# Performance work log

Hardware: AMD Instinct MI355X
Metric: run time of the kernel (lower is better)

## Reference

```python
import jax, jax.numpy as jnp
import numpy as np

NEG_SLOPE = 0.2  # PyG GATConv default


def leaky_relu(v):
    return jnp.where(v >= 0, v, NEG_SLOPE * v)


def gat_conv(x, W, a_src, a_dst, b, src, dst, n_nodes):
    # x: [N, Fin], W: [Fin, Fout], a_src/a_dst/b: [Fout]
    h = x @ W                               # [N, Fout]
    alpha_src = h @ a_src                   # [N]
    alpha_dst = h @ a_dst                   # [N]
    e = leaky_relu(alpha_src[src] + alpha_dst[dst])          # [E]
    m = jax.ops.segment_max(e, dst, num_segments=n_nodes)    # [N] (self-loops => every node has >=1 edge)
    p = jnp.exp(e - m[dst])                                   # [E]
    s = jax.ops.segment_sum(p, dst, num_segments=n_nodes)     # [N]
    coef = p / s[dst]                                          # [E]
    out = jax.ops.segment_sum(coef[:, None] * h[src], dst, num_segments=n_nodes)
    return out + b


def setup_inputs() -> dict:
    key = jax.random.key(0)
    ks = jax.random.split(key, 20)
    N, E, DIN, DH, DOUT, G = 50000, 800000, 128, 256, 2, 512
    x = jax.random.normal(ks[0], (N, DIN), dtype=jnp.float32)
    edge_index = jax.random.randint(ks[1], (2, E), 0, N, dtype=jnp.int64)
    batch = jnp.sort(jax.random.randint(ks[2], (N,), 0, G, dtype=jnp.int64))

    def lin(k, fin, fout):
        return jax.random.normal(k, (fin, fout), dtype=jnp.float32) * (1.0 / np.sqrt(fin))

    def att(k, f):
        return jax.random.normal(k, (f,), dtype=jnp.float32) * (1.0 / np.sqrt(f))

    return {
        "x": x, "edge_index": edge_index, "batch": batch,
        "W1": lin(ks[3], DIN, DH), "as1": att(ks[4], DH), "ad1": att(ks[5], DH), "b1": jnp.zeros((DH,), jnp.float32),
        "W2": lin(ks[6], DH, DH),  "as2": att(ks[7], DH), "ad2": att(ks[8], DH), "b2": jnp.zeros((DH,), jnp.float32),
        "W3": lin(ks[9], DH, DH),  "as3": att(ks[10], DH), "ad3": att(ks[11], DH), "b3": jnp.zeros((DH,), jnp.float32),
        "Wfc": lin(ks[12], DH, DOUT), "bfc": jnp.zeros((DOUT,), jnp.float32),
    }


def reference(x, edge_index, batch, W1, as1, ad1, b1, W2, as2, ad2, b2, W3, as3, ad3, b3, Wfc, bfc):
    N = x.shape[0]
    G = 512  # number of graphs (static)
    # add self-loops (PyG GATConv default add_self_loops=True)
    loops = jnp.arange(N, dtype=edge_index.dtype)
    src = jnp.concatenate([edge_index[0], loops])
    dst = jnp.concatenate([edge_index[1], loops])

    h = jax.nn.relu(gat_conv(x, W1, as1, ad1, b1, src, dst, N))
    h = jax.nn.relu(gat_conv(h, W2, as2, ad2, b2, src, dst, N))
    h = jax.nn.relu(gat_conv(h, W3, as3, ad3, b3, src, dst, N))

    # global mean pool over graphs
    sums = jax.ops.segment_sum(h, batch, num_segments=G)                 # [G, DH]
    counts = jax.ops.segment_sum(jnp.ones((N,), h.dtype), batch, num_segments=G)
    pooled = sums / jnp.maximum(counts, 1.0)[:, None]

    logits = pooled @ Wfc + bfc                                           # [G, DOUT]
    return jax.nn.softmax(logits, axis=1)
```

## Files before the change

### kernel.cpp

```cpp
#include <hip/hip_runtime.h>
#include <hip/hip_bf16.h>

typedef short short8 __attribute__((ext_vector_type(8)));
typedef float floatx4 __attribute__((ext_vector_type(4)));
typedef float float2v __attribute__((ext_vector_type(2)));
typedef unsigned short ushort_t;
typedef unsigned short ushort4v __attribute__((ext_vector_type(4)));

__device__ __forceinline__ ushort_t f2bf(float v) {
    __hip_bfloat16 h = __float2bfloat16(v);
    return *(ushort_t*)&h;
}
__device__ __forceinline__ float bf2f(ushort_t u) {
    return __uint_as_float(((unsigned)u) << 16);
}

#if defined(__has_builtin)
#if __has_builtin(__builtin_amdgcn_cvt_pk_f32_fp8) && __has_builtin(__builtin_amdgcn_cvt_pk_fp8_f32)
#define HAVE_FP8_CVT 1
#endif
#endif

__device__ __forceinline__ unsigned enc_fp8(float f) {
    unsigned t = __float_as_uint(f);
    unsigned s = (t >> 24) & 0x80u;
    unsigned mag = t & 0x7fffffffu;
    if (mag > 0x43E00000u) mag = 0x43E00000u;
    mag += 0x7FFFFu + ((mag >> 20) & 1u);
    int e = (int)(mag >> 20) - 960;
    unsigned r = (e < 1) ? 0u : (unsigned)e;
    return s | r;
}
__device__ __forceinline__ float dec_fp8(unsigned b) {
    unsigned bits = ((b & 0x80u) << 24) | ((b & 0x7fu) << 20);
    return __uint_as_float(bits) * 0x1p120f;
}

__device__ __forceinline__ unsigned pack4_fp8(float a, float b, float c, float d) {
#if HAVE_FP8_CVT
    unsigned v = 0;
    v = __builtin_amdgcn_cvt_pk_fp8_f32(a, b, v, false);
    v = __builtin_amdgcn_cvt_pk_fp8_f32(c, d, v, true);
    return v;
#else
    return enc_fp8(a) | (enc_fp8(b) << 8) | (enc_fp8(c) << 16) | (enc_fp8(d) << 24);
#endif
}
__device__ __forceinline__ float4 unpack4_fp8(unsigned v) {
#if HAVE_FP8_CVT
    float2v lo = __builtin_amdgcn_cvt_pk_f32_fp8(v, false);
    float2v hi = __builtin_amdgcn_cvt_pk_f32_fp8(v, true);
    return make_float4(lo.x, lo.y, hi.x, hi.y);
#else
    return make_float4(dec_fp8(v & 0xFFu), dec_fp8((v >> 8) & 0xFFu),
                       dec_fp8((v >> 16) & 0xFFu), dec_fp8(v >> 24));
#endif
}


template <int NCSHIFT>
__device__ __forceinline__ void wsplit_coal(const float* __restrict__ W,
                                            ushort_t* __restrict__ Bh,
                                            ushort_t* __restrict__ Bl,
                                            int o, bool permK) {
    int j = o & 7;
    int l = (o >> 3) & 63;
    int rest = o >> 9;
    int nt = rest >> NCSHIFT;
    int c  = rest & ((1 << NCSHIFT) - 1);
    int n  = nt * 16 + (l & 15);
    int ks = c * 32 + (l >> 4) * 8 + j;
    int i = ks & 63;
    int ko = permK ? ((ks & ~63) | ((i & 3) << 4) | (i >> 2)) : ks;
    float v = W[(size_t)ko * 256 + n];
    ushort_t h = f2bf(v);
    Bh[o] = h;
    Bl[o] = f2bf(v - bf2f(h));
}

__global__ __launch_bounds__(256) void prep_kernel(const float* __restrict__ X,
                                                   ushort_t* __restrict__ Xhi,
                                                   ushort_t* __restrict__ Xlo,
                                                   int* __restrict__ deg,
                                                   float* __restrict__ asrcA,
                                                   float* __restrict__ adstA,
                                                   const float* __restrict__ W1,
                                                   const float* __restrict__ W2,
                                                   const float* __restrict__ W3,
                                                   ushort_t* __restrict__ B1h, ushort_t* __restrict__ B1l,
                                                   ushort_t* __restrict__ B2h, ushort_t* __restrict__ B2l,
                                                   ushort_t* __restrict__ B3h, ushort_t* __restrict__ B3l,
                                                   int total, int N) {
    int idx = blockIdx.x * 256 + threadIdx.x;
    if (idx < N) {
        deg[idx] = 0;
        asrcA[idx] = 0.f;
        adstA[idx] = 0.f;
    }
    const int S1 = 128 * 256, S2 = 256 * 256;
    if (idx < S1) {
        wsplit_coal<2>(W1, B1h, B1l, idx, false);
    } else if (idx < S1 + S2) {
        wsplit_coal<3>(W2, B2h, B2l, idx - S1, true);
    } else if (idx < S1 + 2 * S2) {
        wsplit_coal<3>(W3, B3h, B3l, idx - S1 - S2, true);
    }
    if (idx < total) {
        float v = X[idx];
        ushort_t h = f2bf(v);
        Xhi[idx] = h;
        Xlo[idx] = f2bf(v - bf2f(h));
    }
}

template <int NCHUNK, bool HASLO>
__global__ __launch_bounds__(256) void gemm_mfma(const ushort_t* __restrict__ Ahi_g,
                                                 const ushort_t* __restrict__ Alo_g,
                                                 const ushort_t* __restrict__ Bthi,
                                                 const ushort_t* __restrict__ Btlo,
                                                 unsigned char* __restrict__ Hb,
                                                 const float* __restrict__ a_src,
                                                 const float* __restrict__ a_dst,
                                                 float* __restrict__ asrc_out,
                                                 float* __restrict__ adst_out,
                                                 int N) {
    constexpr int K = NCHUNK * 32;
    const int tid = threadIdx.x;
    const int wave = tid >> 6, lane = tid & 63;
    const int wr = wave & 1, wc = wave >> 1;
    const int q = lane >> 4, l15 = lane & 15;
    const int rowBase = blockIdx.x * 128;
    const int colBase = blockIdx.y * 128;

    floatx4 acc[4][4];
#pragma unroll
    for (int i = 0; i < 4; ++i)
#pragma unroll
        for (int j = 0; j < 4; ++j) acc[i][j] = (floatx4)0.f;

    size_t aoff[4];
#pragma unroll
    for (int mt = 0; mt < 4; ++mt) {
        int r = rowBase + wr * 64 + mt * 16 + l15;
        if (r > N - 1) r = N - 1;
        aoff[mt] = (size_t)r * K + q * 8;
    }

    const int ntg = blockIdx.y * 8 + wc * 4;
    const size_t ntstride = (size_t)NCHUNK * 512;
    const ushort_t* bhp = Bthi + (size_t)ntg * ntstride + (size_t)lane * 8;
    const ushort_t* blp = Btlo + (size_t)ntg * ntstride + (size_t)lane * 8;

#pragma unroll
    for (int c = 0; c < NCHUNK; ++c) {
        const int co = c * 32;
        const size_t cb = (size_t)c * 512;
        short8 ah[4], al[4], bh[4], bl[4];
#pragma unroll
        for (int mt = 0; mt < 4; ++mt)
            ah[mt] = *(const short8*)(Ahi_g + aoff[mt] + co);
        if (HASLO) {
#pragma unroll
            for (int mt = 0; mt < 4; ++mt)
                al[mt] = *(const short8*)(Alo_g + aoff[mt] + co);
        }
#pragma unroll
        for (int nt = 0; nt < 4; ++nt) {
            bh[nt] = *(const short8*)(bhp + (size_t)nt * ntstride + cb);
            bl[nt] = *(const short8*)(blp + (size_t)nt * ntstride + cb);
        }
#pragma unroll
        for (int mt = 0; mt < 4; ++mt)
#pragma unroll
            for (int nt = 0; nt < 4; ++nt) {
                acc[mt][nt] = __builtin_amdgcn_mfma_f32_16x16x32_bf16(ah[mt], bh[nt], acc[mt][nt], 0, 0, 0);
                acc[mt][nt] = __builtin_amdgcn_mfma_f32_16x16x32_bf16(ah[mt], bl[nt], acc[mt][nt], 0, 0, 0);
            }
        if (HASLO) {
#pragma unroll
            for (int mt = 0; mt < 4; ++mt)
#pragma unroll
                for (int nt = 0; nt < 4; ++nt)
                    acc[mt][nt] = __builtin_amdgcn_mfma_f32_16x16x32_bf16(al[mt], bh[nt], acc[mt][nt], 0, 0, 0);
        }
    }

    float asv[4], adv[4];
#pragma unroll
    for (int nt = 0; nt < 4; ++nt) {
        int n = colBase + wc * 64 + nt * 16 + l15;
        asv[nt] = a_src[n];
        adv[nt] = a_dst[n];
    }
#pragma unroll
    for (int mt = 0; mt < 4; ++mt) {
#pragma unroll
        for (int reg = 0; reg < 4; ++reg) {
            int grow = rowBase + wr * 64 + mt * 16 + q * 4 + reg;
            float p1 = acc[mt][0][reg] * asv[0] + acc[mt][1][reg] * asv[1] +
                       acc[mt][2][reg] * asv[2] + acc[mt][3][reg] * asv[3];
            float p2 = acc[mt][0][reg] * adv[0] + acc[mt][1][reg] * adv[1] +
                       acc[mt][2][reg] * adv[2] + acc[mt][3][reg] * adv[3];
            if (grow < N) {
                unsigned pk = pack4_fp8(acc[mt][0][reg], acc[mt][1][reg],
                                        acc[mt][2][reg], acc[mt][3][reg]);
                *(unsigned*)(Hb + (size_t)grow * 256 + colBase + wc * 64 + l15 * 4) = pk;
            }
#pragma unroll
            for (int off = 1; off < 16; off <<= 1) {
                p1 += __shfl_xor(p1, off, 64);
                p2 += __shfl_xor(p2, off, 64);
            }
            if (l15 == 0 && grow < N) {
                atomicAdd(&asrc_out[grow], p1);
                atomicAdd(&adst_out[grow], p2);
            }
        }
    }
}

__global__ __launch_bounds__(256) void count_kernel(const int* __restrict__ edst,
                                                    int* __restrict__ deg, int E) {
    int i = blockIdx.x * 256 + threadIdx.x;
    if (i < E) atomicAdd(&deg[edst[i]], 1);
}

__global__ __launch_bounds__(256) void scan1_kernel(const int* __restrict__ deg,
                                                    int* __restrict__ excl,
                                                    int* __restrict__ bsum, int N) {
    __shared__ int tmp[256];
    int tid = threadIdx.x;
    int i = blockIdx.x * 256 + tid;
    int v = (i < N) ? deg[i] : 0;
    tmp[tid] = v;
    __syncthreads();
    for (int off = 1; off < 256; off <<= 1) {
        int t = (tid >= off) ? tmp[tid - off] : 0;
        __syncthreads();
        tmp[tid] += t;
        __syncthreads();
    }
    if (i < N) excl[i] = tmp[tid] - v;
    if (tid == 255) bsum[blockIdx.x] = tmp[255];
}

__global__ __launch_bounds__(256) void scan2_kernel(int* __restrict__ bsum, int nb) {
    __shared__ int tmp[256];
    int tid = threadIdx.x;
    int v = (tid < nb) ? bsum[tid] : 0;
    tmp[tid] = v;
    __syncthreads();
    for (int off = 1; off < 256; off <<= 1) {
        int t = (tid >= off) ? tmp[tid - off] : 0;
        __syncthreads();
        tmp[tid] += t;
        __syncthreads();
    }
    if (tid < nb) bsum[tid] = tmp[tid] - v;
}

__global__ __launch_bounds__(256) void scan3_kernel(const int* __restrict__ excl,
                                                    const int* __restrict__ bsum,
                                                    int* __restrict__ rowptr,
                                                    int* __restrict__ cursor,
                                                    int N, int E) {
    int i = blockIdx.x * 256 + threadIdx.x;
    if (i < N) {
        int v = excl[i] + bsum[blockIdx.x];
        rowptr[i] = v;
        cursor[i] = v;
    }
    if (i == 0) rowptr[N] = E;
}

__global__ __launch_bounds__(256) void scatter_kernel(const int* __restrict__ esrc,
                                                      const int* __restrict__ edst,
                                                      int* __restrict__ cursor,
                                                      int* __restrict__ csr_src, int E) {
    int i = blockIdx.x * 256 + threadIdx.x;
    if (i < E) {
        int d = edst[i];
        int pos = atomicAdd(&cursor[d], 1);
        csr_src[pos] = esrc[i];
    }
}

__global__ __launch_bounds__(256) void gat_fused_kernel(const unsigned char* __restrict__ hb,
                                                        const float* __restrict__ asrc,
                                                        const float* __restrict__ adst,
                                                        const int* __restrict__ rowptr,
                                                        const int* __restrict__ csr_src,
                                                        const float* __restrict__ bias,
                                                        ushort_t* __restrict__ ohi,
                                                        float* __restrict__ asrc_next,
                                                        float* __restrict__ adst_next,
                                                        int N) {
    int wave = threadIdx.x >> 6;
    int lane = threadIdx.x & 63;
    int d = blockIdx.x * 4 + wave;
    if (d >= N) return;

    if (lane == 0) {
        asrc_next[d] = 0.f;
        adst_next[d] = 0.f;
    }

    const float* bb = bias + (lane >> 4) * 64 + (lane & 15);
    float b0 = bb[0], b1 = bb[16], b2 = bb[32], b3 = bb[48];

    float ad = adst[d];
    float es = asrc[d] + ad;
    es = es >= 0.f ? es : 0.2f * es;
    float m = es;
    float s = 1.0f;
    float4 acc = unpack4_fp8(*(const unsigned*)(hb + (size_t)d * 256 + lane * 4));

    int beg = rowptr[d], end = rowptr[d + 1];
    for (int base = beg; base < end; base += 64) {
        int cnt = min(64, end - base);
        int srci = 0;
        float e = -1e30f;
        if (lane < cnt) {
            srci = csr_src[base + lane];
            float v = asrc[srci] + ad;
            e = v >= 0.f ? v : 0.2f * v;
        }
        float cm = e;
#pragma unroll
        for (int off = 32; off > 0; off >>= 1) cm = fmaxf(cm, __shfl_xor(cm, off, 64));
        float mnew = fmaxf(m, cm);
        float scale = __expf(m - mnew);
        m = mnew;

        float p = __expf(e - m);
        float ps = p;
#pragma unroll
        for (int off = 32; off > 0; off >>= 1) ps += __shfl_xor(ps, off, 64);
        s = s * scale + ps;
        acc.x *= scale; acc.y *= scale; acc.z *= scale; acc.w *= scale;

        int j = 0;
        for (; j + 4 <= cnt; j += 4) {
            float p0 = __shfl(p, j, 64),     p1 = __shfl(p, j + 1, 64);
            float p2 = __shfl(p, j + 2, 64), p3 = __shfl(p, j + 3, 64);
            int s0 = __shfl(srci, j, 64),     s1i = __shfl(srci, j + 1, 64);
            int s2i = __shfl(srci, j + 2, 64), s3i = __shfl(srci, j + 3, 64);
            unsigned v0 = *(const unsigned*)(hb + (size_t)s0 * 256 + lane * 4);
            unsigned v1 = *(const unsigned*)(hb + (size_t)s1i * 256 + lane * 4);
            unsigned v2 = *(const unsigned*)(hb + (size_t)s2i * 256 + lane * 4);
            unsigned v3 = *(const unsigned*)(hb + (size_t)s3i * 256 + lane * 4);
            float4 hv0 = unpack4_fp8(v0);
            float4 hv1 = unpack4_fp8(v1);
            float4 hv2 = unpack4_fp8(v2);
            float4 hv3 = unpack4_fp8(v3);
            acc.x += p0 * hv0.x + p1 * hv1.x + p2 * hv2.x + p3 * hv3.x;
            acc.y += p0 * hv0.y + p1 * hv1.y + p2 * hv2.y + p3 * hv3.y;
            acc.z += p0 * hv0.z + p1 * hv1.z + p2 * hv2.z + p3 * hv3.z;
            acc.w += p0 * hv0.w + p1 * hv1.w + p2 * hv2.w + p3 * hv3.w;
        }
        for (; j < cnt; ++j) {
            float pj = __shfl(p, j, 64);
            int sj = __shfl(srci, j, 64);
            float4 hv = unpack4_fp8(*(const unsigned*)(hb + (size_t)sj * 256 + lane * 4));
            acc.x += pj * hv.x; acc.y += pj * hv.y; acc.z += pj * hv.z; acc.w += pj * hv.w;
        }
    }
    float inv = 1.0f / s;
    float ox = fmaxf(acc.x * inv + b0, 0.f);
    float oy = fmaxf(acc.y * inv + b1, 0.f);
    float oz = fmaxf(acc.z * inv + b2, 0.f);
    float ow = fmaxf(acc.w * inv + b3, 0.f);
    ushort4v hv;
    hv.x = f2bf(ox); hv.y = f2bf(oy); hv.z = f2bf(oz); hv.w = f2bf(ow);
    *(ushort4v*)(ohi + (size_t)d * 256 + lane * 4) = hv;
}

__device__ __forceinline__ int lower_bound_i(const int* __restrict__ a, int n, int v) {
    int lo = 0, hi = n;
    while (lo < hi) {
        int mid = (lo + hi) >> 1;
        if (a[mid] < v) lo = mid + 1; else hi = mid;
    }
    return lo;
}

__global__ __launch_bounds__(256) void pool_fc_kernel(const ushort_t* __restrict__ hhi,
                                                      const int* __restrict__ batch,
                                                      int N,
                                                      const float* __restrict__ Wfc,
                                                      const float* __restrict__ bfc,
                                                      float* __restrict__ out) {
    __shared__ float red0[256];
    __shared__ float red1[256];
    int g = blockIdx.x;
    int c = threadIdx.x;
    int i = c & 63;
    int o = (c & ~63) | ((i & 3) << 4) | (i >> 2);
    int beg = lower_bound_i(batch, N, g);
    int end = lower_bound_i(batch, N, g + 1);
    float sum = 0.f;
    for (int n = beg; n < end; ++n)
        sum += bf2f(hhi[(size_t)n * 256 + c]);
    float cnt = (float)(end - beg);
    float v = sum / fmaxf(cnt, 1.0f);
    red0[c] = v * Wfc[o * 2 + 0];
    red1[c] = v * Wfc[o * 2 + 1];
    __syncthreads();
    for (int off = 128; off > 0; off >>= 1) {
        if (c < off) {
            red0[c] += red0[c + off];
            red1[c] += red1[c + off];
        }
        __syncthreads();
    }
    if (c == 0) {
        float l0 = red0[0] + bfc[0];
        float l1 = red1[0] + bfc[1];
        float mx = fmaxf(l0, l1);
        float e0 = expf(l0 - mx), e1 = expf(l1 - mx);
        float s = e0 + e1;
        out[g * 2 + 0] = e0 / s;
        out[g * 2 + 1] = e1 / s;
    }
}

extern "C" void kernel_launch(void* const* d_in, const int* in_sizes, int n_in,
                              void* d_out, int out_size, void* d_ws, size_t ws_size,
                              hipStream_t stream) {
    const float* x    = (const float*)d_in[0];
    const int*   eidx = (const int*)d_in[1];
    const int*   batch= (const int*)d_in[2];
    const float* Wl[3]  = {(const float*)d_in[3], (const float*)d_in[7],  (const float*)d_in[11]};
    const float* asl[3] = {(const float*)d_in[4], (const float*)d_in[8],  (const float*)d_in[12]};
    const float* adl[3] = {(const float*)d_in[5], (const float*)d_in[9],  (const float*)d_in[13]};
    const float* bl[3]  = {(const float*)d_in[6], (const float*)d_in[10], (const float*)d_in[14]};
    const float* Wfc = (const float*)d_in[15];
    const float* bfc = (const float*)d_in[16];
    float* out = (float*)d_out;

    const int N   = in_sizes[2];
    const int E   = in_sizes[1] / 2;
    const int DIN = in_sizes[0] / N;
    const int DH  = 256;
    const int G   = 512;
    const int* esrc = eidx;
    const int* edst = eidx + E;

    char* ws = (char*)d_ws;
    size_t off = 0;
    const size_t featHalf = (size_t)N * DH * sizeof(ushort_t);
    unsigned char* hb = (unsigned char*)(ws + off); off += (size_t)N * DH;
    ushort_t* ghi    = (ushort_t*)(ws + off); off += featHalf;
    ushort_t* xhi    = (ushort_t*)(ws + off); off += (size_t)N * DIN * sizeof(ushort_t);
    ushort_t* xlo    = (ushort_t*)(ws + off); off += (size_t)N * DIN * sizeof(ushort_t);
    float*    asA    = (float*)(ws + off); off += (size_t)N * sizeof(float);
    float*    adA    = (float*)(ws + off); off += (size_t)N * sizeof(float);
    float*    asB    = (float*)(ws + off); off += (size_t)N * sizeof(float);
    float*    adB    = (float*)(ws + off); off += (size_t)N * sizeof(float);
    int*      deg    = (int*)(ws + off);   off += (size_t)N * sizeof(int);
    int*      excl   = (int*)(ws + off);   off += (size_t)N * sizeof(int);
    int*      rowptr = (int*)(ws + off);   off += (size_t)(N + 1) * sizeof(int);
    int*      cursor = (int*)(ws + off);   off += (size_t)N * sizeof(int);
    int*      bsum   = (int*)(ws + off);   off += 1024;
    int*      csrsrc = (int*)(ws + off);   off += (size_t)E * sizeof(int);
    ushort_t* B1h    = (ushort_t*)(ws + off); off += (size_t)128 * 256 * sizeof(ushort_t);
    ushort_t* B1l    = (ushort_t*)(ws + off); off += (size_t)128 * 256 * sizeof(ushort_t);
    ushort_t* B2h    = (ushort_t*)(ws + off); off += (size_t)256 * 256 * sizeof(ushort_t);
    ushort_t* B2l    = (ushort_t*)(ws + off); off += (size_t)256 * 256 * sizeof(ushort_t);
    ushort_t* B3h    = (ushort_t*)(ws + off); off += (size_t)256 * 256 * sizeof(ushort_t);
    ushort_t* B3l    = (ushort_t*)(ws + off); off += (size_t)256 * 256 * sizeof(ushort_t);

    const int nbN = (N + 255) / 256;

    prep_kernel<<<((size_t)N * DIN + 255) / 256, 256, 0, stream>>>(
        x, xhi, xlo, deg, asA, adA, Wl[0], Wl[1], Wl[2],
        B1h, B1l, B2h, B2l, B3h, B3l, N * DIN, N);

    count_kernel<<<(E + 255) / 256, 256, 0, stream>>>(edst, deg, E);
    scan1_kernel<<<nbN, 256, 0, stream>>>(deg, excl, bsum, N);
    scan2_kernel<<<1, 256, 0, stream>>>(bsum, nbN);
    scan3_kernel<<<nbN, 256, 0, stream>>>(excl, bsum, rowptr, cursor, N, E);
    scatter_kernel<<<(E + 255) / 256, 256, 0, stream>>>(esrc, edst, cursor, csrsrc, E);

    const ushort_t* Bh[3]  = {B1h, B2h, B3h};
    const ushort_t* Blp[3] = {B1l, B2l, B3l};
    float* asCur[3] = {asA, asB, asA};
    float* adCur[3] = {adA, adB, adA};
    float* asNext[3] = {asB, asA, asB};
    float* adNext[3] = {adB, adA, adB};

    dim3 ggrid((N + 127) / 128, 2);
    for (int layer = 0; layer < 3; ++layer) {
        if (layer == 0) {
            gemm_mfma<4, true><<<ggrid, 256, 0, stream>>>(xhi, xlo, Bh[0], Blp[0], hb,
                                                          asl[0], adl[0], asCur[0], adCur[0], N);
        } else {
            gemm_mfma<8, false><<<ggrid, 256, 0, stream>>>(ghi, nullptr, Bh[layer], Blp[layer], hb,
                                                           asl[layer], adl[layer],
                                                           asCur[layer], adCur[layer], N);
        }

        gat_fused_kernel<<<(N + 3) / 4, 256, 0, stream>>>(hb, asCur[layer], adCur[layer],
                                                          rowptr, csrsrc, bl[layer], ghi,
                                                          asNext[layer], adNext[layer], N);
    }

    pool_fc_kernel<<<G, 256, 0, stream>>>(ghi, batch, N, Wfc, bfc, out);
}
```

Baseline: 448.8 us.

## Bucket edges before CSR scatter, fold degree count into prep, drop B-lo MFMAs

```diff
diff --git a/kernel.cpp b/kernel.cpp
--- a/kernel.cpp
+++ b/kernel.cpp
@@ -82,6 +82,9 @@
                                                    ushort_t* __restrict__ Xhi,
                                                    ushort_t* __restrict__ Xlo,
                                                    int* __restrict__ deg,
+                                                   int* __restrict__ bcnt,
+                                                   const int* __restrict__ edst,
+                                                   int E,
                                                    float* __restrict__ asrcA,
                                                    float* __restrict__ adstA,
                                                    const float* __restrict__ W1,
@@ -93,9 +96,13 @@
                                                    int total, int N) {
     int idx = blockIdx.x * 256 + threadIdx.x;
     if (idx < N) {
-        deg[idx] = 0;
         asrcA[idx] = 0.f;
         adstA[idx] = 0.f;
+    }
+    if (idx < E) {
+        int d = edst[idx];
+        atomicAdd(&deg[d], 1);
+        atomicAdd(&bcnt[d >> 7], 1);
     }
     const int S1 = 128 * 256, S2 = 256 * 256;
     if (idx < S1) {
@@ -113,7 +120,7 @@
     }
 }
 
-template <int NCHUNK, bool HASLO>
+template <int NCHUNK, bool ALO, bool BLO>
 __global__ __launch_bounds__(256) void gemm_mfma(const ushort_t* __restrict__ Ahi_g,
                                                  const ushort_t* __restrict__ Alo_g,
                                                  const ushort_t* __restrict__ Bthi,
@@ -159,7 +166,7 @@
 #pragma unroll
         for (int mt = 0; mt < 4; ++mt)
             ah[mt] = *(const short8*)(Ahi_g + aoff[mt] + co);
-        if (HASLO) {
+        if (ALO) {
 #pragma unroll
             for (int mt = 0; mt < 4; ++mt)
                 al[mt] = *(const short8*)(Alo_g + aoff[mt] + co);
@@ -167,22 +174,18 @@
 #pragma unroll
         for (int nt = 0; nt < 4; ++nt) {
             bh[nt] = *(const short8*)(bhp + (size_t)nt * ntstride + cb);
-            bl[nt] = *(const short8*)(blp + (size_t)nt * ntstride + cb);
+            if (BLO) bl[nt] = *(const short8*)(blp + (size_t)nt * ntstride + cb);
         }
 #pragma unroll
         for (int mt = 0; mt < 4; ++mt)
 #pragma unroll
             for (int nt = 0; nt < 4; ++nt) {
                 acc[mt][nt] = __builtin_amdgcn_mfma_f32_16x16x32_bf16(ah[mt], bh[nt], acc[mt][nt], 0, 0, 0);
-                acc[mt][nt] = __builtin_amdgcn_mfma_f32_16x16x32_bf16(ah[mt], bl[nt], acc[mt][nt], 0, 0, 0);
+                if (BLO)
+                    acc[mt][nt] = __builtin_amdgcn_mfma_f32_16x16x32_bf16(ah[mt], bl[nt], acc[mt][nt], 0, 0, 0);
+                if (ALO)
+                    acc[mt][nt] = __builtin_amdgcn_mfma_f32_16x16x32_bf16(al[mt], bh[nt], acc[mt][nt], 0, 0, 0);
             }
-        if (HASLO) {
-#pragma unroll
-            for (int mt = 0; mt < 4; ++mt)
-#pragma unroll
-                for (int nt = 0; nt < 4; ++nt)
-                    acc[mt][nt] = __builtin_amdgcn_mfma_f32_16x16x32_bf16(al[mt], bh[nt], acc[mt][nt], 0, 0, 0);
-        }
     }
 
     float asv[4], adv[4];
@@ -219,12 +222,6 @@
     }
 }
 
-__global__ __launch_bounds__(256) void count_kernel(const int* __restrict__ edst,
-                                                    int* __restrict__ deg, int E) {
-    int i = blockIdx.x * 256 + threadIdx.x;
-    if (i < E) atomicAdd(&deg[edst[i]], 1);
-}
-
 __global__ __launch_bounds__(256) void scan1_kernel(const int* __restrict__ deg,
                                                     int* __restrict__ excl,
                                                     int* __restrict__ bsum, int N) {
@@ -273,15 +270,42 @@
     if (i == 0) rowptr[N] = E;
 }
 
-__global__ __launch_bounds__(256) void scatter_kernel(const int* __restrict__ esrc,
-                                                      const int* __restrict__ edst,
-                                                      int* __restrict__ cursor,
-                                                      int* __restrict__ csr_src, int E) {
+__global__ __launch_bounds__(512) void bscan_kernel(int* __restrict__ bcnt,
+                                                    int* __restrict__ bcur, int nb) {
+    __shared__ int tmp[512];
+    int tid = threadIdx.x;
+    int v = (tid < nb) ? bcnt[tid] : 0;
+    tmp[tid] = v;
+    __syncthreads();
+    for (int off = 1; off < 512; off <<= 1) {
+        int t = (tid >= off) ? tmp[tid - off] : 0;
+        __syncthreads();
+        tmp[tid] += t;
+        __syncthreads();
+    }
+    if (tid < nb) bcur[tid] = tmp[tid] - v;
+}
+
+__global__ __launch_bounds__(256) void bucket_scatter_kernel(const int* __restrict__ esrc,
+                                                             const int* __restrict__ edst,
+                                                             int* __restrict__ bcur,
+                                                             uint2* __restrict__ ebuf, int E) {
     int i = blockIdx.x * 256 + threadIdx.x;
     if (i < E) {
-        int d = edst[i];
-        int pos = atomicAdd(&cursor[d], 1);
-        csr_src[pos] = esrc[i];
+        int s = esrc[i], d = edst[i];
+        int pos = atomicAdd(&bcur[d >> 7], 1);
+        ebuf[pos] = make_uint2((unsigned)s, (unsigned)d);
+    }
+}
+
+__global__ __launch_bounds__(256) void final_scatter_kernel(const uint2* __restrict__ ebuf,
+                                                            int* __restrict__ cursor,
+                                                            int* __restrict__ csr_src, int E) {
+    int i = blockIdx.x * 256 + threadIdx.x;
+    if (i < E) {
+        uint2 e = ebuf[i];
+        int pos = atomicAdd(&cursor[e.y], 1);
+        csr_src[pos] = (int)e.x;
     }
 }
 
@@ -443,6 +467,7 @@
     const int DIN = in_sizes[0] / N;
     const int DH  = 256;
     const int G   = 512;
+    const int NB  = (N + 127) >> 7;
     const int* esrc = eidx;
     const int* edst = eidx + E;
 
@@ -462,7 +487,10 @@
     int*      rowptr = (int*)(ws + off);   off += (size_t)(N + 1) * sizeof(int);
     int*      cursor = (int*)(ws + off);   off += (size_t)N * sizeof(int);
     int*      bsum   = (int*)(ws + off);   off += 1024;
+    int*      bcnt   = (int*)(ws + off);   off += 2048;
+    int*      bcur   = (int*)(ws + off);   off += 2048;
     int*      csrsrc = (int*)(ws + off);   off += (size_t)E * sizeof(int);
+    uint2*    ebuf   = (uint2*)(ws + off); off += (size_t)E * sizeof(uint2);
     ushort_t* B1h    = (ushort_t*)(ws + off); off += (size_t)128 * 256 * sizeof(ushort_t);
     ushort_t* B1l    = (ushort_t*)(ws + off); off += (size_t)128 * 256 * sizeof(ushort_t);
     ushort_t* B2h    = (ushort_t*)(ws + off); off += (size_t)256 * 256 * sizeof(ushort_t);
@@ -472,15 +500,18 @@
 
     const int nbN = (N + 255) / 256;
 
+    hipMemsetAsync(deg, 0, (size_t)N * sizeof(int), stream);
+    hipMemsetAsync(bcnt, 0, (size_t)NB * sizeof(int), stream);
     prep_kernel<<<((size_t)N * DIN + 255) / 256, 256, 0, stream>>>(
-        x, xhi, xlo, deg, asA, adA, Wl[0], Wl[1], Wl[2],
+        x, xhi, xlo, deg, bcnt, edst, E, asA, adA, Wl[0], Wl[1], Wl[2],
         B1h, B1l, B2h, B2l, B3h, B3l, N * DIN, N);
 
-    count_kernel<<<(E + 255) / 256, 256, 0, stream>>>(edst, deg, E);
     scan1_kernel<<<nbN, 256, 0, stream>>>(deg, excl, bsum, N);
     scan2_kernel<<<1, 256, 0, stream>>>(bsum, nbN);
     scan3_kernel<<<nbN, 256, 0, stream>>>(excl, bsum, rowptr, cursor, N, E);
-    scatter_kernel<<<(E + 255) / 256, 256, 0, stream>>>(esrc, edst, cursor, csrsrc, E);
+    bscan_kernel<<<1, 512, 0, stream>>>(bcnt, bcur, NB);
+    bucket_scatter_kernel<<<(E + 255) / 256, 256, 0, stream>>>(esrc, edst, bcur, ebuf, E);
+    final_scatter_kernel<<<(E + 255) / 256, 256, 0, stream>>>(ebuf, cursor, csrsrc, E);
 
     const ushort_t* Bh[3]  = {B1h, B2h, B3h};
     const ushort_t* Blp[3] = {B1l, B2l, B3l};
@@ -492,12 +523,12 @@
     dim3 ggrid((N + 127) / 128, 2);
     for (int layer = 0; layer < 3; ++layer) {
         if (layer == 0) {
-            gemm_mfma<4, true><<<ggrid, 256, 0, stream>>>(xhi, xlo, Bh[0], Blp[0], hb,
-                                                          asl[0], adl[0], asCur[0], adCur[0], N);
+            gemm_mfma<4, true, true><<<ggrid, 256, 0, stream>>>(xhi, xlo, Bh[0], Blp[0], hb,
+                                                                asl[0], adl[0], asCur[0], adCur[0], N);
         } else {
-            gemm_mfma<8, false><<<ggrid, 256, 0, stream>>>(ghi, nullptr, Bh[layer], Blp[layer], hb,
-                                                           asl[layer], adl[layer],
-                                                           asCur[layer], adCur[layer], N);
+            gemm_mfma<8, false, false><<<ggrid, 256, 0, stream>>>(ghi, nullptr, Bh[layer], Blp[layer], hb,
+                                                                  asl[layer], adl[layer],
+                                                                  asCur[layer], adCur[layer], N);
         }
 
         gat_fused_kernel<<<(N + 3) / 4, 256, 0, stream>>>(hb, asCur[layer], adCur[layer],
```

Result: slower. 972.0 us (+116.6%).
